# Optimization experiments

Hardware: AMD Instinct MI355X
Metric: run time of the kernel (lower is better)

Reference implementation:

```python
import jax, jax.numpy as jnp
import numpy as np

NODE_F = 8      # node_features
HID = 128       # hidden_dim
HEADS = 8       # nn.MultiheadAttention num_heads
OUT = 256       # output_dim
MAX_ATOMS = 4096  # max_pocket_atoms
NEIGHBOR_RADIUS = 3.0   # _compute_surface_scores neighbor_radius


def setup_inputs() -> dict:
    key = jax.random.key(0)
    ks = jax.random.split(key, 16)
    N, M = 16384, 32
    x = jax.random.normal(ks[0], (N, NODE_F), dtype=jnp.float32)
    pos = jax.random.normal(ks[1], (N, 3), dtype=jnp.float32) * 10.0
    ligand_pos = jax.random.normal(ks[2], (M, 3), dtype=jnp.float32) * 3.0

    def lin(k, fan_in, fan_out):
        return jax.random.normal(k, (fan_in, fan_out), dtype=jnp.float32) / np.sqrt(fan_in)

    return {
        'x': x, 'pos': pos, 'ligand_pos': ligand_pos,
        'W_node': lin(ks[3], NODE_F, HID), 'b_node': jnp.zeros((HID,), jnp.float32),
        'Wq': lin(ks[4], HID, HID), 'bq': jnp.zeros((HID,), jnp.float32),
        'Wk': lin(ks[5], HID, HID), 'bk': jnp.zeros((HID,), jnp.float32),
        'Wv': lin(ks[6], HID, HID), 'bv': jnp.zeros((HID,), jnp.float32),
        'Wo': lin(ks[7], HID, HID), 'bo': jnp.zeros((HID,), jnp.float32),
        'W1': lin(ks[8], HID, OUT), 'b1': jnp.zeros((OUT,), jnp.float32),
        'W2': lin(ks[9], OUT, OUT), 'b2': jnp.zeros((OUT,), jnp.float32),
    }


def _select_binding_site(pos, ligand_pos, k):
    # select_by_binding_site_proximity: distance-to-ligand-center + surface scores, topk
    lig_center = jnp.mean(ligand_pos, axis=0)                       # [3]
    d_lig = jnp.linalg.norm(pos - lig_center, axis=1)               # [N]
    # _compute_surface_scores: cdist(pos,pos) < 3.0, count neighbors (minus self)
    sq = jnp.sum(pos * pos, axis=1)                                 # [N]
    d2 = sq[:, None] + sq[None, :] - 2.0 * (pos @ pos.T)            # [N,N] squared distances
    neighbor_counts = jnp.sum(d2 < NEIGHBOR_RADIUS ** 2, axis=1) - 1
    surface = 1.0 / (neighbor_counts.astype(jnp.float32) + 1.0)
    scores = 1.0 / (1.0 + d_lig / 5.0) + 0.5 * surface
    _, idx = jax.lax.top_k(scores, k)                               # largest=True
    return idx


def reference(x, pos, ligand_pos, W_node, b_node, Wq, bq, Wk, bk, Wv, bv, Wo, bo, W1, b1, W2, b2):
    # N > max_pocket_atoms -> smart selection (adaptive with ligand_pos => binding_site)
    idx = _select_binding_site(pos, ligand_pos, MAX_ATOMS)
    xs = x[idx]                                                     # [K, NODE_F]

    # node embedding (E3 net call fails in the original -> h = node_embedding(x))
    h = xs @ W_node + b_node                                        # [K, HID]

    # MultiheadAttention over the single (batch=None) sequence, eval mode (no dropout)
    K = MAX_ATOMS
    dh = HID // HEADS
    q = (h @ Wq + bq).reshape(K, HEADS, dh).transpose(1, 0, 2)      # [H,K,dh]
    k_ = (h @ Wk + bk).reshape(K, HEADS, dh).transpose(1, 0, 2)
    v = (h @ Wv + bv).reshape(K, HEADS, dh).transpose(1, 0, 2)
    attn = jax.nn.softmax(jnp.einsum('hqd,hkd->hqk', q, k_) / np.sqrt(dh), axis=-1)
    av = jnp.einsum('hqk,hkd->hqd', attn, v).transpose(1, 0, 2).reshape(K, HID)
    h_att = av @ Wo + bo                                            # [K, HID]

    # global mean pool + output projection (Linear-ReLU-Linear)
    pooled = jnp.mean(h_att, axis=0)                                # [HID]
    out = jax.nn.relu(pooled @ W1 + b1) @ W2 + b2                   # [OUT]
    return out
```

## Files before the change

kernel.cpp:

```cpp
#include <hip/hip_runtime.h>
#include <cstdint>
#include <cstddef>

#define NPTS 16384
#define KSEL 4096
#define HIDDEN 128
#define NHEADS 8
#define DHEAD 16
#define OUTD 256
#define NSLICE 4
#define FCAP 131072
#define LCAP 512
#define TAU 0.2f

typedef __attribute__((ext_vector_type(8))) short bf16x8;
typedef __attribute__((ext_vector_type(4))) float f32x4;
typedef __attribute__((ext_vector_type(16))) float f32x16;

#if defined(__has_builtin)
#if __has_builtin(__builtin_amdgcn_exp2f)
#define E2(x) __builtin_amdgcn_exp2f(x)
#endif
#endif
#ifndef E2
#define E2(x) exp2f(x)
#endif

constexpr size_t OFF_PA    = 1024;
constexpr size_t OFF_PB    = OFF_PA  + (size_t)NPTS*32;
constexpr size_t OFF_SQ    = OFF_PB  + (size_t)NPTS*32;
constexpr size_t OFF_DL    = OFF_SQ  + (size_t)NPTS*4;
constexpr size_t OFF_CNT   = OFF_DL  + (size_t)NPTS*4;
constexpr size_t OFF_NFLAG = OFF_CNT + (size_t)NPTS*4;
constexpr size_t OFF_FLG   = OFF_NFLAG + 1024;
constexpr size_t OFF_SEL   = OFF_FLG + (size_t)FCAP*4;
constexpr size_t SZ_PK     = (size_t)NHEADS*KSEL*32*2;
constexpr size_t OFF_QPK   = OFF_SEL + (size_t)KSEL*4;
constexpr size_t OFF_KPK   = OFF_QPK + SZ_PK;
constexpr size_t OFF_V     = OFF_KPK + SZ_PK;
constexpr size_t OFF_LP    = OFF_V  + (size_t)KSEL*HIDDEN*4;
constexpr size_t OFF_RL    = OFF_LP + (size_t)NHEADS*KSEL*NSLICE*4;
constexpr size_t OFF_WP    = OFF_RL + (size_t)NHEADS*KSEL*4;
constexpr size_t OFF_PAV   = OFF_WP + (size_t)NHEADS*KSEL*NSLICE*4;

__device__ __forceinline__ unsigned short f2bf(float f) {
    union { float f; unsigned u; } v; v.f = f;
    unsigned r = v.u + 0x7fffu + ((v.u >> 16) & 1u);
    return (unsigned short)(r >> 16);
}
__device__ __forceinline__ float bf2f(unsigned short h) {
    union { unsigned u; float f; } v; v.u = ((unsigned)h) << 16;
    return v.f;
}

__global__ void __launch_bounds__(256) k_prep(const float* __restrict__ pos, const float* __restrict__ lig, int M,
                       unsigned short* __restrict__ pa, unsigned short* __restrict__ pb,
                       float* __restrict__ sq, float* __restrict__ dl, float* __restrict__ pav,
                       int* __restrict__ cnt, unsigned int* __restrict__ nfl) {
    __shared__ float ls[128];
    __shared__ float ctr[3];
    int tid = threadIdx.x;
    if (blockIdx.x == 0) {
        if (tid < HIDDEN) pav[tid] = 0.f;
        if (tid < 2) nfl[tid] = 0;
    }
    for (int i = tid; i < 3 * M; i += 256) ls[i] = lig[i];
    __syncthreads();
    if (tid < 3) {
        float s = 0.f;
        for (int i = 0; i < M; i++) s += ls[i * 3 + tid];
        ctr[tid] = s / (float)M;
    }
    __syncthreads();
    int i = blockIdx.x * 256 + tid;
    cnt[i] = 0;
    float x = pos[i*3+0], y = pos[i*3+1], z = pos[i*3+2];
    float s = (x*x + y*y) + z*z;
    sq[i] = s;
    float dx = x - ctr[0], dy = y - ctr[1], dz = z - ctr[2];
    dl[i] = sqrtf((dx*dx + dy*dy) + dz*dz);
    unsigned short xh = f2bf(x); float xr = bf2f(xh); float xl = x - xr;
    unsigned short yh = f2bf(y); float yr = bf2f(yh); float yl = y - yr;
    unsigned short zh = f2bf(z); float zr = bf2f(zh); float zl = z - zr;
    unsigned short xlb = f2bf(xl), ylb = f2bf(yl), zlb = f2bf(zl);
    unsigned short xhA = f2bf(-2.f*xr), xlA = f2bf(-2.f*xl);
    unsigned short yhA = f2bf(-2.f*yr), ylA = f2bf(-2.f*yl);
    unsigned short zhA = f2bf(-2.f*zr), zlA = f2bf(-2.f*zl);
    float sm9 = s - 9.0f;
    unsigned short sihA = f2bf(sm9);
    unsigned short silA = f2bf(sm9 - bf2f(sihA));
    unsigned short sih = f2bf(s);
    unsigned short sil = f2bf(s - bf2f(sih));
    unsigned short one = f2bf(1.0f);
    union { unsigned short s[16]; float4 f[2]; } A, B;
    A.s[0]=xhA; A.s[1]=xhA; A.s[2]=xlA;
    A.s[3]=yhA; A.s[4]=yhA; A.s[5]=ylA;
    A.s[6]=zhA; A.s[7]=zhA; A.s[8]=zlA;
    A.s[9]=xlA; A.s[10]=ylA; A.s[11]=zlA;
    A.s[12]=sihA; A.s[13]=silA; A.s[14]=one; A.s[15]=one;
    B.s[0]=xh;  B.s[1]=xlb;  B.s[2]=xh;
    B.s[3]=yh;  B.s[4]=ylb;  B.s[5]=yh;
    B.s[6]=zh;  B.s[7]=zlb;  B.s[8]=zh;
    B.s[9]=xlb; B.s[10]=ylb; B.s[11]=zlb;
    B.s[12]=one; B.s[13]=one; B.s[14]=sih; B.s[15]=sil;
    float4* pad = (float4*)(pa + (size_t)i * 16);
    pad[0] = A.f[0]; pad[1] = A.f[1];
    float4* pbd = (float4*)(pb + (size_t)i * 16);
    pbd[0] = B.f[0]; pbd[1] = B.f[1];
}

__global__ void __launch_bounds__(256) k_neighbor(
        const unsigned short* __restrict__ pa, const unsigned short* __restrict__ pb,
        int* __restrict__ cnt, unsigned int* __restrict__ flg, unsigned int* __restrict__ nflag) {
    __shared__ unsigned short js[256 * 24];
    __shared__ unsigned int fbuf[LCAP];
    __shared__ unsigned int fcnt, fbase;
    int tid = threadIdx.x;
    if (tid == 0) fcnt = 0;
    int lane = tid & 63, w = tid >> 6;
    int half = lane >> 5, il = lane & 31;
    int i = blockIdx.x * 128 + w * 32 + il;
    bf16x8 bfrag = *(const bf16x8*)(pb + (size_t)i * 16 + half * 8);
    int jb0 = blockIdx.y * 1024;
    int acc = 0;
    const f32x16 czero = {0.f,0.f,0.f,0.f,0.f,0.f,0.f,0.f,0.f,0.f,0.f,0.f,0.f,0.f,0.f,0.f};
    for (int chv = 0; chv < 4; chv++) {
        int jb = jb0 + chv * 256;
        __syncthreads();
        {
            const float4* src = (const float4*)(pa + (size_t)(jb + tid) * 16);
            float4 v0 = src[0], v1 = src[1];
            float4* dst = (float4*)&js[tid * 24];
            dst[0] = v0; dst[1] = v1;
        }
        __syncthreads();
        #pragma unroll 2
        for (int t = 0; t < 8; t++) {
            bf16x8 afrag = *(const bf16x8*)&js[(t * 32 + il) * 24 + half * 8];
            f32x16 c = __builtin_amdgcn_mfma_f32_32x32x16_bf16(afrag, bfrag, czero, 0, 0, 0);
            int cs = 0;
            #pragma unroll
            for (int r = 0; r < 16; r++) cs += (c[r] < -TAU);
            acc += cs;
            float a0 = fminf(fabsf(c[0]),  fabsf(c[1]));
            float a1 = fminf(fabsf(c[2]),  fabsf(c[3]));
            float a2 = fminf(fabsf(c[4]),  fabsf(c[5]));
            float a3 = fminf(fabsf(c[6]),  fabsf(c[7]));
            float a4 = fminf(fabsf(c[8]),  fabsf(c[9]));
            float a5 = fminf(fabsf(c[10]), fabsf(c[11]));
            float a6 = fminf(fabsf(c[12]), fabsf(c[13]));
            float a7 = fminf(fabsf(c[14]), fabsf(c[15]));
            float b0 = fminf(a0, a1), b1 = fminf(a2, a3);
            float b2 = fminf(a4, a5), b3 = fminf(a6, a7);
            float mn = fminf(fminf(b0, b1), fminf(b2, b3));
            if (mn <= TAU) {
                int jt = jb + t * 32;
                #pragma unroll
                for (int r = 0; r < 16; r++) {
                    float d = c[r];
                    if (d >= -TAU && d < TAU) {
                        int j = jt + (r & 3) + 8 * (r >> 2) + 4 * half;
                        unsigned xx = atomicAdd(&fcnt, 1u);
                        if (xx < LCAP) fbuf[xx] = ((unsigned)i << 14) | (unsigned)j;
                    }
                }
            }
        }
    }
    acc += __shfl_xor(acc, 32);
    if (half == 0) atomicAdd(&cnt[i], acc);
    __syncthreads();
    if (tid == 0) {
        unsigned cf = fcnt; if (cf > LCAP) cf = LCAP;
        fcnt = cf;
        fbase = atomicAdd(nflag, cf);
    }
    __syncthreads();
    unsigned cf = fcnt, fb = fbase;
    for (unsigned xx = tid; xx < cf; xx += 256) {
        unsigned di = fb + xx;
        if (di < FCAP) flg[di] = fbuf[xx];
    }
}

__global__ void __launch_bounds__(256) k_fixup(const float* __restrict__ pos, const float* __restrict__ sq,
        const unsigned int* __restrict__ flg, const unsigned int* __restrict__ nflag,
        int* __restrict__ cnt) {
    int nf = (int)*nflag; if (nf > FCAP) nf = FCAP;
    for (int idx = blockIdx.x * 256 + threadIdx.x; idx < nf; idx += gridDim.x * 256) {
        unsigned pr = flg[idx];
        int i = (int)((pr >> 14) & 16383u), j = (int)(pr & 16383u);
        float xi = pos[i*3+0], yi = pos[i*3+1], zi = pos[i*3+2];
        float xj = pos[j*3+0], yj = pos[j*3+1], zj = pos[j*3+2];
        float dot = fmaf(xi, xj, fmaf(yi, yj, zi * zj));
        float d2 = (sq[i] + sq[j]) - 2.0f * dot;
        if (d2 < 9.0f) atomicAdd(&cnt[i], 1);
    }
}

__global__ void __launch_bounds__(1024) k_select(const float* __restrict__ dl, const int* __restrict__ cnt,
                                                 int* __restrict__ sel) {
    __shared__ unsigned int sk[NPTS];
    __shared__ int histw[16][256];
    __shared__ int hist[256];
    __shared__ int scan2[256];
    __shared__ unsigned int s_prefix;
    __shared__ int s_rem, s_eqtot, s_nout, s_digit, s_cgt;
    int tid = threadIdx.x;
    int lane = tid & 63, wid = tid >> 6;
    for (int i = tid; i < NPTS; i += 1024) {
        float score = 1.0f / (1.0f + dl[i] / 5.0f) + 0.5f * (1.0f / (float)cnt[i]);
        unsigned int u = __float_as_uint(score);
        sk[i] = u ^ ((u & 0x80000000u) ? 0xFFFFFFFFu : 0x80000000u);
    }
    if (tid == 0) { s_prefix = 0; s_rem = KSEL; s_nout = 0; s_eqtot = 0; }
    __syncthreads();
    for (int p = 0; p < 4; p++) {
        int sh = 24 - 8 * p;
        for (int b = tid; b < 4096; b += 1024) ((int*)histw)[b] = 0;
        __syncthreads();
        unsigned int pref = s_prefix;
        int shp = (p == 0) ? 0 : (32 - 8 * p);
        for (int i = tid; i < NPTS; i += 1024) {
            unsigned int key = sk[i];
            bool m = (p == 0) || ((key >> shp) == pref);
            if (m) atomicAdd(&histw[wid][(key >> sh) & 255], 1);
        }
        __syncthreads();
        if (tid < 256) {
            int s = 0;
            #pragma unroll
            for (int w2 = 0; w2 < 16; w2++) s += histw[w2][tid];
            hist[tid] = s;
            scan2[tid] = s;
        }
        __syncthreads();
        for (int off = 1; off < 256; off <<= 1) {
            int v = 0;
            if (tid < 256) { v = scan2[tid]; if (tid + off < 256) v += scan2[tid + off]; }
            __syncthreads();
            if (tid < 256) scan2[tid] = v;
            __syncthreads();
        }
        int rem = s_rem;
        if (tid < 256) {
            int hi = scan2[tid];
            int lo = hi - hist[tid];
            if (hi >= rem && lo < rem) { s_digit = tid; s_cgt = lo; }
        }
        __syncthreads();
        if (tid == 0) {
            s_prefix = (s_prefix << 8) | (unsigned int)s_digit;
            s_rem = rem - s_cgt;
            if (p == 3) s_eqtot = hist[s_digit];
        }
        __syncthreads();
    }
    unsigned int T = s_prefix;
    int need_eq = s_rem;
    for (int i = tid; i < NPTS; i += 1024) {
        bool cond = (sk[i] > T);
        unsigned long long bal = __ballot(cond);
        if (bal) {
            int leader = __ffsll((long long)bal) - 1;
            int b0 = 0;
            if (lane == leader) b0 = atomicAdd(&s_nout, __popcll(bal));
            b0 = __shfl(b0, leader);
            if (cond) {
                unsigned long long lower = bal & ((1ULL << lane) - 1ULL);
                sel[b0 + __popcll(lower)] = i;
            }
        }
    }
    __syncthreads();
    if (s_eqtot == need_eq) {
        for (int i = tid; i < NPTS; i += 1024) {
            bool cond = (sk[i] == T);
            unsigned long long bal = __ballot(cond);
            if (bal) {
                int leader = __ffsll((long long)bal) - 1;
                int b0 = 0;
                if (lane == leader) b0 = atomicAdd(&s_nout, __popcll(bal));
                b0 = __shfl(b0, leader);
                if (cond) {
                    unsigned long long lower = bal & ((1ULL << lane) - 1ULL);
                    sel[b0 + __popcll(lower)] = i;
                }
            }
        }
    } else {
        for (int i = tid; i < NPTS; i += 1024) {
            if (sk[i] == T) {
                int rank = 0;
                for (int j = 0; j < i; j++) rank += (sk[j] == T);
                if (rank < need_eq) sel[atomicAdd(&s_nout, 1)] = i;
            }
        }
    }
}

__device__ __forceinline__ void proj4(const float hs[4][HIDDEN], const float* __restrict__ W,
                                      float b, int d, float* acc) {
    #pragma unroll
    for (int r = 0; r < 4; r++) acc[r] = b;
    for (int c = 0; c < HIDDEN; c += 4) {
        float w0 = W[(c+0)*HIDDEN+d], w1 = W[(c+1)*HIDDEN+d], w2 = W[(c+2)*HIDDEN+d], w3 = W[(c+3)*HIDDEN+d];
        #pragma unroll
        for (int r = 0; r < 4; r++) {
            float4 h4 = *(const float4*)&hs[r][c];
            float a = acc[r];
            a = fmaf(h4.x, w0, a); a = fmaf(h4.y, w1, a); a = fmaf(h4.z, w2, a); a = fmaf(h4.w, w3, a);
            acc[r] = a;
        }
    }
}

__global__ void __launch_bounds__(128) k_qkv(const float* __restrict__ x, const int* __restrict__ sel,
        const float* __restrict__ Wn, const float* __restrict__ bn,
        const float* __restrict__ Wq, const float* __restrict__ bq,
        const float* __restrict__ Wk, const float* __restrict__ bk,
        const float* __restrict__ Wv, const float* __restrict__ bv,
        unsigned short* __restrict__ qpk, unsigned short* __restrict__ kpk,
        float* __restrict__ vg) {
    __shared__ float xs[4][8];
    __shared__ __align__(16) float hs[4][HIDDEN];
    int d = threadIdx.x;
    int r0 = blockIdx.x * 4;
    if (d < 32) { int rr = d >> 3, cc = d & 7; xs[rr][cc] = x[(size_t)sel[r0 + rr] * 8 + cc]; }
    __syncthreads();
    {
        float wn[8];
        #pragma unroll
        for (int c = 0; c < 8; c++) wn[c] = Wn[c * HIDDEN + d];
        float b = bn[d];
        #pragma unroll
        for (int r = 0; r < 4; r++) {
            float a = b;
            #pragma unroll
            for (int c = 0; c < 8; c++) a = fmaf(xs[r][c], wn[c], a);
            hs[r][d] = a;
        }
    }
    __syncthreads();
    int hh = d >> 4, dd = d & 15;
    float acc[4];
    proj4(hs, Wq, bq[d], d, acc);
    #pragma unroll
    for (int r = 0; r < 4; r++) {
        float val = acc[r] * 0.36067376022224085f;
        unsigned short hi = f2bf(val);
        unsigned short lo = f2bf(val - bf2f(hi));
        size_t idx = ((size_t)(hh * KSEL) + r0 + r) * 32 + dd;
        qpk[idx] = hi; qpk[idx + 16] = lo;
    }
    proj4(hs, Wk, bk[d], d, acc);
    #pragma unroll
    for (int r = 0; r < 4; r++) {
        float val = acc[r];
        unsigned short hi = f2bf(val);
        unsigned short lo = f2bf(val - bf2f(hi));
        size_t idx = ((size_t)(hh * KSEL) + r0 + r) * 32 + dd;
        kpk[idx] = hi; kpk[idx + 16] = lo;
    }
    proj4(hs, Wv, bv[d], d, acc);
    #pragma unroll
    for (int r = 0; r < 4; r++) vg[(size_t)(r0+r)*HIDDEN + d] = acc[r];
}

__global__ void __launch_bounds__(512) k_attn_l(
        const unsigned short* __restrict__ qpk, const unsigned short* __restrict__ kpk,
        float* __restrict__ lp) {
    __shared__ unsigned short smem[256 * 40];
    int tid = threadIdx.x;
    int ks = blockIdx.x, yg = blockIdx.y, h = blockIdx.z;
    size_t hb = (size_t)h * KSEL;
    int lane = tid & 63, w = tid >> 6;
    int n = lane & 15, g = lane >> 4;
    int q0w = yg * 128 + w * 16;
    bf16x8 afrag = *(const bf16x8*)(qpk + (hb + q0w + n) * 32 + g * 8);
    float l0 = 0.f, l1 = 0.f, l2 = 0.f, l3 = 0.f;
    int b1off = (g & 1) * 8;
    int b2off = 16 + g * 8;
    for (int kc = 0; kc < 4; kc++) {
        __syncthreads();
        {
            int row = tid >> 1, hf = tid & 1;
            int krow = ks * 1024 + kc * 256 + row;
            const float4* src = (const float4*)(kpk + (hb + krow) * 32 + hf * 16);
            float4 a0 = src[0], a1 = src[1];
            float4* dst = (float4*)&smem[row * 40 + hf * 16];
            dst[0] = a0; dst[1] = a1;
        }
        __syncthreads();
        #pragma unroll 4
        for (int t = 0; t < 16; t++) {
            const unsigned short* rowp = &smem[(t * 16 + n) * 40];
            bf16x8 b1 = *(const bf16x8*)(rowp + b1off);
            bf16x8 b2 = {0,0,0,0,0,0,0,0};
            if (g < 2) b2 = *(const bf16x8*)(rowp + b2off);
            f32x4 c = {0.f, 0.f, 0.f, 0.f};
            c = __builtin_amdgcn_mfma_f32_16x16x32_bf16(afrag, b1, c, 0, 0, 0);
            c = __builtin_amdgcn_mfma_f32_16x16x32_bf16(afrag, b2, c, 0, 0, 0);
            l0 += E2(c[0]); l1 += E2(c[1]); l2 += E2(c[2]); l3 += E2(c[3]);
        }
    }
    #pragma unroll
    for (int m = 1; m < 16; m <<= 1) {
        l0 += __shfl_xor(l0, m); l1 += __shfl_xor(l1, m);
        l2 += __shfl_xor(l2, m); l3 += __shfl_xor(l3, m);
    }
    if (n == 0) {
        size_t base = (hb + q0w + g * 4) * NSLICE + ks;
        lp[base]            = l0; lp[base + NSLICE]     = l1;
        lp[base + 2*NSLICE] = l2; lp[base + 3*NSLICE]   = l3;
    }
}

__global__ void __launch_bounds__(512) k_attn_w(
        const unsigned short* __restrict__ qpk, const unsigned short* __restrict__ kpk,
        const float* __restrict__ lp, float* __restrict__ wp) {
    __shared__ unsigned short smem[256 * 40];
    __shared__ float rls[256];
    int tid = threadIdx.x;
    int qs = blockIdx.x, yg = blockIdx.y, h = blockIdx.z;
    size_t hb = (size_t)h * KSEL;
    int lane = tid & 63, w = tid >> 6;
    int n = lane & 15, g = lane >> 4;
    int j0w = yg * 128 + w * 16;
    bf16x8 afrag = *(const bf16x8*)(kpk + (hb + j0w + n) * 32 + g * 8);
    float w0 = 0.f, w1 = 0.f, w2 = 0.f, w3 = 0.f;
    int b1off = (g & 1) * 8;
    int b2off = 16 + g * 8;
    for (int qc = 0; qc < 4; qc++) {
        __syncthreads();
        {
            int row = tid >> 1, hf = tid & 1;
            int qrow = qs * 1024 + qc * 256 + row;
            const float4* src = (const float4*)(qpk + (hb + qrow) * 32 + hf * 16);
            float4 a0 = src[0], a1 = src[1];
            float4* dst = (float4*)&smem[row * 40 + hf * 16];
            dst[0] = a0; dst[1] = a1;
            if (hf == 0) {
                float4 p = ((const float4*)lp)[hb + qrow];
                rls[row] = 1.0f / ((p.x + p.y) + (p.z + p.w));
            }
        }
        __syncthreads();
        #pragma unroll 4
        for (int t = 0; t < 16; t++) {
            const unsigned short* rowp = &smem[(t * 16 + n) * 40];
            bf16x8 b1 = *(const bf16x8*)(rowp + b1off);
            bf16x8 b2 = {0,0,0,0,0,0,0,0};
            if (g < 2) b2 = *(const bf16x8*)(rowp + b2off);
            f32x4 c = {0.f, 0.f, 0.f, 0.f};
            c = __builtin_amdgcn_mfma_f32_16x16x32_bf16(afrag, b1, c, 0, 0, 0);
            c = __builtin_amdgcn_mfma_f32_16x16x32_bf16(afrag, b2, c, 0, 0, 0);
            float rv = rls[t * 16 + n];
            w0 = fmaf(E2(c[0]), rv, w0); w1 = fmaf(E2(c[1]), rv, w1);
            w2 = fmaf(E2(c[2]), rv, w2); w3 = fmaf(E2(c[3]), rv, w3);
        }
    }
    #pragma unroll
    for (int m = 1; m < 16; m <<= 1) {
        w0 += __shfl_xor(w0, m); w1 += __shfl_xor(w1, m);
        w2 += __shfl_xor(w2, m); w3 += __shfl_xor(w3, m);
    }
    if (n == 0) {
        size_t base = (hb + j0w + g * 4) * NSLICE + qs;
        wp[base]            = w0; wp[base + NSLICE]     = w1;
        wp[base + 2*NSLICE] = w2; wp[base + 3*NSLICE]   = w3;
    }
}

__global__ void __launch_bounds__(256) k_colsum(const float* __restrict__ wp, const float* __restrict__ vg,
        float* __restrict__ pav, unsigned int* __restrict__ done,
        const float* __restrict__ Wo, const float* __restrict__ bo,
        const float* __restrict__ W1, const float* __restrict__ b1,
        const float* __restrict__ W2, const float* __restrict__ b2,
        float* __restrict__ out) {
    __shared__ float wl[NHEADS][32];
    __shared__ float red[128];
    __shared__ int isLast;
    int tid = threadIdx.x;
    int j0 = blockIdx.x * 32;
    {
        int h = tid >> 5, jl = tid & 31;
        float4 p = ((const float4*)wp)[(size_t)h * KSEL + j0 + jl];
        wl[h][jl] = (p.x + p.y) + (p.z + p.w);
    }
    __syncthreads();
    int d = tid & 127, g = tid >> 7;
    int h = d >> 4;
    float acc = 0.f;
    for (int jl = g * 16; jl < g * 16 + 16; jl++)
        acc = fmaf(wl[h][jl], vg[(size_t)(j0 + jl) * HIDDEN + d], acc);
    if (g == 1) red[d] = acc;
    __syncthreads();
    if (g == 0) atomicAdd(&pav[d], (acc + red[d]) * (1.0f / (float)KSEL));
    __threadfence();
    __syncthreads();
    if (tid == 0) isLast = (atomicAdd(done, 1u) == (unsigned)(KSEL / 32 - 1));
    __syncthreads();
    if (!isLast) return;
    __shared__ float pv[HIDDEN];
    __shared__ float sp[HIDDEN];
    __shared__ float st[OUTD];
    if (tid < HIDDEN) pv[tid] = atomicAdd(&pav[tid], 0.0f);
    __syncthreads();
    if (tid < HIDDEN) {
        float a = bo[tid];
        for (int c = 0; c < HIDDEN; c++) a = fmaf(pv[c], Wo[c * HIDDEN + tid], a);
        sp[tid] = a;
    }
    __syncthreads();
    {
        float a = b1[tid];
        for (int c = 0; c < HIDDEN; c++) a = fmaf(sp[c], W1[c * OUTD + tid], a);
        st[tid] = fmaxf(a, 0.f);
    }
    __syncthreads();
    {
        float o = b2[tid];
        for (int c = 0; c < OUTD; c++) o = fmaf(st[c], W2[c * OUTD + tid], o);
        out[tid] = o;
    }
}

extern "C" void kernel_launch(void* const* d_in, const int* in_sizes, int n_in,
                              void* d_out, int out_size, void* d_ws, size_t ws_size,
                              hipStream_t stream) {
    (void)n_in; (void)out_size; (void)ws_size;
    const float* x   = (const float*)d_in[0];
    const float* pos = (const float*)d_in[1];
    const float* lig = (const float*)d_in[2];
    const float* Wn  = (const float*)d_in[3];
    const float* bn  = (const float*)d_in[4];
    const float* Wq  = (const float*)d_in[5];
    const float* bq  = (const float*)d_in[6];
    const float* Wk  = (const float*)d_in[7];
    const float* bk  = (const float*)d_in[8];
    const float* Wv  = (const float*)d_in[9];
    const float* bv  = (const float*)d_in[10];
    const float* Wo  = (const float*)d_in[11];
    const float* bo  = (const float*)d_in[12];
    const float* W1  = (const float*)d_in[13];
    const float* b1  = (const float*)d_in[14];
    const float* W2  = (const float*)d_in[15];
    const float* b2  = (const float*)d_in[16];
    int M = in_sizes[2] / 3;

    char* ws = (char*)d_ws;
    unsigned short* pa  = (unsigned short*)(ws + OFF_PA);
    unsigned short* pb  = (unsigned short*)(ws + OFF_PB);
    float*          sq  = (float*)(ws + OFF_SQ);
    float*          dl  = (float*)(ws + OFF_DL);
    int*            cnt = (int*)  (ws + OFF_CNT);
    unsigned int*   nfl = (unsigned int*)(ws + OFF_NFLAG);
    unsigned int*   flg = (unsigned int*)(ws + OFF_FLG);
    int*            sel = (int*)  (ws + OFF_SEL);
    unsigned short* qpk = (unsigned short*)(ws + OFF_QPK);
    unsigned short* kpk = (unsigned short*)(ws + OFF_KPK);
    float*          vg  = (float*)(ws + OFF_V);
    float*          lp  = (float*)(ws + OFF_LP);
    float*          wp  = (float*)(ws + OFF_WP);
    float*          pav = (float*)(ws + OFF_PAV);

    hipLaunchKernelGGL(k_prep,     dim3(64),       dim3(256),  0, stream, pos, lig, M, pa, pb, sq, dl, pav, cnt, nfl);
    hipLaunchKernelGGL(k_neighbor, dim3(128, 16),  dim3(256),  0, stream, pa, pb, cnt, flg, nfl);
    hipLaunchKernelGGL(k_fixup,    dim3(32),       dim3(256),  0, stream, pos, sq, flg, nfl, cnt);
    hipLaunchKernelGGL(k_select,   dim3(1),        dim3(1024), 0, stream, dl, cnt, sel);
    hipLaunchKernelGGL(k_qkv,      dim3(KSEL/4),   dim3(128),  0, stream, x, sel, Wn, bn, Wq, bq, Wk, bk, Wv, bv, qpk, kpk, vg);
    hipLaunchKernelGGL(k_attn_l,   dim3(4, 32, 8), dim3(512),  0, stream, qpk, kpk, lp);
    hipLaunchKernelGGL(k_attn_w,   dim3(4, 32, 8), dim3(512),  0, stream, qpk, kpk, lp, wp);
    hipLaunchKernelGGL(k_colsum,   dim3(KSEL/32),  dim3(256),  0, stream, wp, vg, pav, nfl + 1,
                       Wo, bo, W1, b1, W2, b2, (float*)d_out);
}
```

Before: 265.1 us.

## Parallelize top-k selection with a 16-block global histogram and last-block finish

Replaces the single-block four-pass 8-bit radix select with a 16-block pass that builds a 13-bit histogram of score keys in shared memory and merges it into a global histogram. The last block to finish, detected with an atomic counter, scans the histogram to find the threshold bin, emits all keys above it, and ranks candidates in that bin with an O(C^2) shared-memory comparison. This is meant to cut the serial radix passes and barrier-heavy scans of the old kernel. The cost is global atomics, extra zeroing in k_prep, and reliance on candidate counts in the threshold bin staying small.

Result: slower. 309.0 us (+16.6%).

```diff
diff --git a/kernel.cpp b/kernel.cpp
--- a/kernel.cpp
+++ b/kernel.cpp
@@ -12,6 +12,8 @@
 #define FCAP 131072
 #define LCAP 512
 #define TAU 0.2f
+#define SBITS 13
+#define SBINS 8192
 
 typedef __attribute__((ext_vector_type(8))) short bf16x8;
 typedef __attribute__((ext_vector_type(4))) float f32x4;
@@ -42,6 +44,8 @@
 constexpr size_t OFF_RL    = OFF_LP + (size_t)NHEADS*KSEL*NSLICE*4;
 constexpr size_t OFF_WP    = OFF_RL + (size_t)NHEADS*KSEL*4;
 constexpr size_t OFF_PAV   = OFF_WP + (size_t)NHEADS*KSEL*NSLICE*4;
+constexpr size_t OFF_GH    = OFF_RL;
+constexpr size_t OFF_GK    = OFF_RL + 32768;
 
 __device__ __forceinline__ unsigned short f2bf(float f) {
     union { float f; unsigned u; } v; v.f = f;
@@ -56,13 +60,18 @@
 __global__ void __launch_bounds__(256) k_prep(const float* __restrict__ pos, const float* __restrict__ lig, int M,
                        unsigned short* __restrict__ pa, unsigned short* __restrict__ pb,
                        float* __restrict__ sq, float* __restrict__ dl, float* __restrict__ pav,
-                       int* __restrict__ cnt, unsigned int* __restrict__ nfl) {
+                       int* __restrict__ cnt, unsigned int* __restrict__ nfl,
+                       unsigned int* __restrict__ ghist) {
     __shared__ float ls[128];
     __shared__ float ctr[3];
     int tid = threadIdx.x;
     if (blockIdx.x == 0) {
         if (tid < HIDDEN) pav[tid] = 0.f;
-        if (tid < 2) nfl[tid] = 0;
+        if (tid < 3) nfl[tid] = 0;
+    }
+    {
+        int gz = blockIdx.x * 256 + tid;
+        if (gz < SBINS) ghist[gz] = 0;
     }
     for (int i = tid; i < 3 * M; i += 256) ls[i] = lig[i];
     __syncthreads();
@@ -199,102 +208,113 @@
 }
 
 __global__ void __launch_bounds__(1024) k_select(const float* __restrict__ dl, const int* __restrict__ cnt,
-                                                 int* __restrict__ sel) {
-    __shared__ unsigned int sk[NPTS];
-    __shared__ int histw[16][256];
-    __shared__ int hist[256];
-    __shared__ int scan2[256];
-    __shared__ unsigned int s_prefix;
-    __shared__ int s_rem, s_eqtot, s_nout, s_digit, s_cgt;
-    int tid = threadIdx.x;
-    int lane = tid & 63, wid = tid >> 6;
+        unsigned int* __restrict__ ghist, unsigned int* __restrict__ sdone,
+        unsigned int* __restrict__ gkeys, int* __restrict__ sel) {
+    __shared__ int lh[SBINS];
+    __shared__ int wsum[16];
+    __shared__ int s_bin, s_rem, s_nout, s_ncand, isLast;
+    __shared__ unsigned int ck[4096];
+    __shared__ unsigned short cidx[4096];
+    int tid = threadIdx.x, lane = tid & 63, wid = tid >> 6;
+    for (int b = tid; b < SBINS; b += 1024) lh[b] = 0;
+    __syncthreads();
+    {
+        int i = blockIdx.x * 1024 + tid;
+        float score = 1.0f / (1.0f + dl[i] / 5.0f) + 0.5f * (1.0f / (float)cnt[i]);
+        unsigned int u = __float_as_uint(score);
+        unsigned int key = u ^ ((u & 0x80000000u) ? 0xFFFFFFFFu : 0x80000000u);
+        atomicAdd(&lh[key >> (32 - SBITS)], 1);
+    }
+    __syncthreads();
+    for (int b = tid; b < SBINS; b += 1024) {
+        int v = lh[b];
+        if (v) atomicAdd(&ghist[b], (unsigned)v);
+    }
+    __threadfence();
+    __syncthreads();
+    if (tid == 0) isLast = (atomicAdd(sdone, 1u) == 15u);
+    __syncthreads();
+    if (!isLast) return;
+    int h8[8]; int tot = 0;
+    #pragma unroll
+    for (int q = 0; q < 8; q++) { h8[q] = (int)atomicAdd(&ghist[tid * 8 + q], 0u); tot += h8[q]; }
+    int s = tot;
+    #pragma unroll
+    for (int off = 1; off < 64; off <<= 1) {
+        int v = __shfl_down(s, off);
+        if (lane + off < 64) s += v;
+    }
+    if (lane == 0) wsum[wid] = s;
+    __syncthreads();
+    if (tid == 0) {
+        int acc2 = 0;
+        for (int w2 = 15; w2 >= 0; w2--) { int t2 = wsum[w2]; wsum[w2] = acc2; acc2 += t2; }
+        s_nout = 0; s_ncand = 0;
+    }
+    __syncthreads();
+    {
+        int after = wsum[wid] + (s - tot);
+        int prev = after;
+        #pragma unroll
+        for (int q = 7; q >= 0; q--) {
+            int cur = prev + h8[q];
+            if (cur >= KSEL && prev < KSEL) { s_bin = tid * 8 + q; s_rem = KSEL - prev; }
+            prev = cur;
+        }
+    }
+    __syncthreads();
+    int T13 = s_bin, rem = s_rem;
     for (int i = tid; i < NPTS; i += 1024) {
         float score = 1.0f / (1.0f + dl[i] / 5.0f) + 0.5f * (1.0f / (float)cnt[i]);
         unsigned int u = __float_as_uint(score);
-        sk[i] = u ^ ((u & 0x80000000u) ? 0xFFFFFFFFu : 0x80000000u);
-    }
-    if (tid == 0) { s_prefix = 0; s_rem = KSEL; s_nout = 0; s_eqtot = 0; }
-    __syncthreads();
-    for (int p = 0; p < 4; p++) {
-        int sh = 24 - 8 * p;
-        for (int b = tid; b < 4096; b += 1024) ((int*)histw)[b] = 0;
-        __syncthreads();
-        unsigned int pref = s_prefix;
-        int shp = (p == 0) ? 0 : (32 - 8 * p);
-        for (int i = tid; i < NPTS; i += 1024) {
-            unsigned int key = sk[i];
-            bool m = (p == 0) || ((key >> shp) == pref);
-            if (m) atomicAdd(&histw[wid][(key >> sh) & 255], 1);
-        }
-        __syncthreads();
-        if (tid < 256) {
-            int s = 0;
-            #pragma unroll
-            for (int w2 = 0; w2 < 16; w2++) s += histw[w2][tid];
-            hist[tid] = s;
-            scan2[tid] = s;
-        }
-        __syncthreads();
-        for (int off = 1; off < 256; off <<= 1) {
-            int v = 0;
-            if (tid < 256) { v = scan2[tid]; if (tid + off < 256) v += scan2[tid + off]; }
-            __syncthreads();
-            if (tid < 256) scan2[tid] = v;
-            __syncthreads();
-        }
-        int rem = s_rem;
-        if (tid < 256) {
-            int hi = scan2[tid];
-            int lo = hi - hist[tid];
-            if (hi >= rem && lo < rem) { s_digit = tid; s_cgt = lo; }
-        }
-        __syncthreads();
-        if (tid == 0) {
-            s_prefix = (s_prefix << 8) | (unsigned int)s_digit;
-            s_rem = rem - s_cgt;
-            if (p == 3) s_eqtot = hist[s_digit];
-        }
-        __syncthreads();
-    }
-    unsigned int T = s_prefix;
-    int need_eq = s_rem;
-    for (int i = tid; i < NPTS; i += 1024) {
-        bool cond = (sk[i] > T);
-        unsigned long long bal = __ballot(cond);
+        unsigned int key = u ^ ((u & 0x80000000u) ? 0xFFFFFFFFu : 0x80000000u);
+        gkeys[i] = key;
+        int bin = (int)(key >> (32 - SBITS));
+        bool take = bin > T13;
+        unsigned long long bal = __ballot(take);
         if (bal) {
             int leader = __ffsll((long long)bal) - 1;
             int b0 = 0;
             if (lane == leader) b0 = atomicAdd(&s_nout, __popcll(bal));
             b0 = __shfl(b0, leader);
-            if (cond) {
-                unsigned long long lower = bal & ((1ULL << lane) - 1ULL);
-                sel[b0 + __popcll(lower)] = i;
+            if (take) sel[b0 + __popcll(bal & ((1ULL << lane) - 1ULL))] = i;
+        }
+        bool cand = (bin == T13);
+        unsigned long long cb = __ballot(cand);
+        if (cb) {
+            int leader = __ffsll((long long)cb) - 1;
+            int c0 = 0;
+            if (lane == leader) c0 = atomicAdd(&s_ncand, __popcll(cb));
+            c0 = __shfl(c0, leader);
+            if (cand) {
+                int pos = c0 + __popcll(cb & ((1ULL << lane) - 1ULL));
+                if (pos < 4096) { ck[pos] = key; cidx[pos] = (unsigned short)i; }
             }
         }
     }
     __syncthreads();
-    if (s_eqtot == need_eq) {
-        for (int i = tid; i < NPTS; i += 1024) {
-            bool cond = (sk[i] == T);
-            unsigned long long bal = __ballot(cond);
-            if (bal) {
-                int leader = __ffsll((long long)bal) - 1;
-                int b0 = 0;
-                if (lane == leader) b0 = atomicAdd(&s_nout, __popcll(bal));
-                b0 = __shfl(b0, leader);
-                if (cond) {
-                    unsigned long long lower = bal & ((1ULL << lane) - 1ULL);
-                    sel[b0 + __popcll(lower)] = i;
-                }
+    int C = s_ncand;
+    if (C <= 4096) {
+        for (int c = tid; c < C; c += 1024) {
+            unsigned int ki = ck[c]; int ii = (int)cidx[c];
+            int rank = 0;
+            for (int j = 0; j < C; j++) {
+                unsigned int kj = ck[j];
+                rank += (int)((kj > ki) || (kj == ki && (int)cidx[j] < ii));
             }
+            if (rank < rem) sel[atomicAdd(&s_nout, 1)] = ii;
         }
     } else {
         for (int i = tid; i < NPTS; i += 1024) {
-            if (sk[i] == T) {
-                int rank = 0;
-                for (int j = 0; j < i; j++) rank += (sk[j] == T);
-                if (rank < need_eq) sel[atomicAdd(&s_nout, 1)] = i;
+            unsigned int ki = gkeys[i];
+            if ((int)(ki >> (32 - SBITS)) != T13) continue;
+            int rank = 0;
+            for (int j = 0; j < NPTS; j++) {
+                unsigned int kj = gkeys[j];
+                if ((int)(kj >> (32 - SBITS)) != T13) continue;
+                rank += (int)((kj > ki) || (kj == ki && j < i));
             }
+            if (rank < rem) sel[atomicAdd(&s_nout, 1)] = i;
         }
     }
 }
@@ -564,11 +584,13 @@
     float*          lp  = (float*)(ws + OFF_LP);
     float*          wp  = (float*)(ws + OFF_WP);
     float*          pav = (float*)(ws + OFF_PAV);
-
-    hipLaunchKernelGGL(k_prep,     dim3(64),       dim3(256),  0, stream, pos, lig, M, pa, pb, sq, dl, pav, cnt, nfl);
+    unsigned int*   ghist = (unsigned int*)(ws + OFF_GH);
+    unsigned int*   gkeys = (unsigned int*)(ws + OFF_GK);
+
+    hipLaunchKernelGGL(k_prep,     dim3(64),       dim3(256),  0, stream, pos, lig, M, pa, pb, sq, dl, pav, cnt, nfl, ghist);
     hipLaunchKernelGGL(k_neighbor, dim3(128, 16),  dim3(256),  0, stream, pa, pb, cnt, flg, nfl);
     hipLaunchKernelGGL(k_fixup,    dim3(32),       dim3(256),  0, stream, pos, sq, flg, nfl, cnt);
-    hipLaunchKernelGGL(k_select,   dim3(1),        dim3(1024), 0, stream, dl, cnt, sel);
+    hipLaunchKernelGGL(k_select,   dim3(16),       dim3(1024), 0, stream, dl, cnt, ghist, nfl + 2, gkeys, sel);
     hipLaunchKernelGGL(k_qkv,      dim3(KSEL/4),   dim3(128),  0, stream, x, sel, Wn, bn, Wq, bq, Wk, bk, Wv, bv, qpk, kpk, vg);
     hipLaunchKernelGGL(k_attn_l,   dim3(4, 32, 8), dim3(512),  0, stream, qpk, kpk, lp);
     hipLaunchKernelGGL(k_attn_w,   dim3(4, 32, 8), dim3(512),  0, stream, qpk, kpk, lp, wp);
```
